# Performance work log

Measured on AMD Instinct MI355X. Metric: run time of the kernel, lower is better.

The kernel has to match this reference:

```python
import jax, jax.numpy as jnp
import numpy as np

K_CENTERS = 10
G_CENTERS = 2
EPS = 1e-12  # tf.math.l2_normalize epsilon


def setup_inputs() -> dict:
    key = jax.random.key(0)
    k1, k2, k3 = jax.random.split(key, 3)
    B, H, W, D = 16, 16, 64, 512
    KC = K_CENTERS + G_CENTERS
    feat = jax.random.normal(k1, (B, H, W, D), dtype=jnp.float32)
    cluster_score = jax.random.normal(k2, (B, H, W, KC), dtype=jnp.float32)
    cluster = jax.random.normal(k3, (KC, D), dtype=jnp.float32)
    return {"feat": feat, "cluster_score": cluster_score, "cluster": cluster}


def reference(feat, cluster_score, cluster):
    B, H, W, D = feat.shape
    KC = cluster.shape[0]
    # Softmax over clusters (stable)
    A = jax.nn.softmax(cluster_score, axis=-1)            # [B,H,W,KC]
    # Flatten spatial dims: sum_{s} A[b,s,k] * (feat[b,s,d] - cluster[k,d])
    Af = A.reshape(B, H * W, KC)
    ff = feat.reshape(B, H * W, D)
    # = einsum(A, feat) - (sum_s A)[b,k] * cluster[k,d]  (avoids [B,S,KC,D] intermediate)
    cluster_res = jnp.einsum('bsk,bsd->bkd', Af, ff) - Af.sum(axis=1)[..., None] * cluster[None]
    # GhostVLAD: keep only real clusters
    cluster_res = cluster_res[:, :K_CENTERS, :]           # [B,K,D]
    # L2 normalize over feature dim
    sq = jnp.sum(cluster_res * cluster_res, axis=-1, keepdims=True)
    cluster_l2 = cluster_res * jax.lax.rsqrt(jnp.maximum(sq, EPS))
    return cluster_l2.reshape(B, K_CENTERS * D)
```

## Files before the change

kernel.cpp:

```cpp
#include <hip/hip_runtime.h>
#include <hip/hip_bf16.h>


#define B_   16
#define S_   1024
#define D_   512
#define KC_  12
#define K_   10
#define CH_  16
#define SCH_ (S_ / CH_)
#define NT1  512
#define NPAR 4

__global__ __launch_bounds__(NT1) void vlad_accum(
    const float* __restrict__ feat, const float* __restrict__ score,
    float* __restrict__ part, float* __restrict__ asum_part)
{
    const int bid = blockIdx.x;
    const int b = bid / CH_, c = bid % CH_;
    const int s0 = c * SCH_;
    const int tid = threadIdx.x;
    const int par = tid >> 7;
    const int col = tid & 127;

    __shared__ float A[SCH_][KC_];
    __shared__ float red[NPAR - 1][K_ * 4][128];

    if (tid < SCH_) {
        const float4* sp = (const float4*)(score + (size_t)(b * S_ + s0 + tid) * KC_);
        const float4 w0 = sp[0], w1 = sp[1], w2 = sp[2];
        float x[KC_] = {w0.x, w0.y, w0.z, w0.w, w1.x, w1.y, w1.z, w1.w,
                        w2.x, w2.y, w2.z, w2.w};
        float m = x[0];
        #pragma unroll
        for (int k = 1; k < KC_; k++) m = fmaxf(m, x[k]);
        float sum = 0.f;
        #pragma unroll
        for (int k = 0; k < KC_; k++) { x[k] = __expf(x[k] - m); sum += x[k]; }
        const float inv = 1.0f / sum;
        #pragma unroll
        for (int k = 0; k < KC_; k++) A[tid][k] = x[k] * inv;
    }
    __syncthreads();

    if (tid < K_) {
        float v = 0.f;
        #pragma unroll
        for (int s = 0; s < SCH_; s++) v += A[s][tid];
        asum_part[(b * CH_ + c) * K_ + tid] = v;
    }

    float acc[K_][4];
    #pragma unroll
    for (int k = 0; k < K_; k++)
        acc[k][0] = acc[k][1] = acc[k][2] = acc[k][3] = 0.f;

    const float4* fp = (const float4*)(feat + (size_t)(b * S_ + s0) * D_) + col;
    #pragma unroll 8
    for (int i = 0; i < SCH_ / NPAR; i++) {
        const int s = NPAR * i + par;
        const float4 v = fp[(size_t)s * (D_ / 4)];
        const float4 a0 = *(const float4*)(&A[s][0]);
        const float4 a1 = *(const float4*)(&A[s][4]);
        const float2 a2 = *(const float2*)(&A[s][8]);
        const float a[K_] = {a0.x, a0.y, a0.z, a0.w, a1.x, a1.y, a1.z, a1.w,
                             a2.x, a2.y};
        #pragma unroll
        for (int k = 0; k < K_; k++) {
            acc[k][0] += a[k] * v.x;
            acc[k][1] += a[k] * v.y;
            acc[k][2] += a[k] * v.z;
            acc[k][3] += a[k] * v.w;
        }
    }

    if (par) {
        float (* const r)[128] = red[par - 1];
        #pragma unroll
        for (int k = 0; k < K_; k++) {
            r[k * 4 + 0][col] = acc[k][0];
            r[k * 4 + 1][col] = acc[k][1];
            r[k * 4 + 2][col] = acc[k][2];
            r[k * 4 + 3][col] = acc[k][3];
        }
    }
    __syncthreads();
    if (!par) {
        float* pp = part + (((size_t)(b * K_) * CH_ + c) * D_) + col * 4;
        #pragma unroll
        for (int k = 0; k < K_; k++) {
            float v0 = acc[k][0], v1 = acc[k][1], v2 = acc[k][2], v3 = acc[k][3];
            #pragma unroll
            for (int p = 0; p < NPAR - 1; p++) {
                v0 += red[p][k * 4 + 0][col];
                v1 += red[p][k * 4 + 1][col];
                v2 += red[p][k * 4 + 2][col];
                v3 += red[p][k * 4 + 3][col];
            }
            *(float4*)(pp + (size_t)k * CH_ * D_) = make_float4(v0, v1, v2, v3);
        }
    }
}

__global__ __launch_bounds__(256) void vlad_final(
    const float* __restrict__ part, const float* __restrict__ asum_part,
    const float* __restrict__ cluster, float* __restrict__ out)
{
    const int b = blockIdx.x / K_;
    const int k = blockIdx.x % K_;
    const int tid = threadIdx.x;
    const int d = tid * 2;

    const float* base = part + ((size_t)(b * K_ + k) * CH_) * D_ + d;
    float s0 = 0.f, s1 = 0.f;
    #pragma unroll 8
    for (int c = 0; c < CH_; c++) {
        const float2 v = *(const float2*)(base + (size_t)c * D_);
        s0 += v.x; s1 += v.y;
    }
    float asv = 0.f;
    #pragma unroll
    for (int c = 0; c < CH_; c++) asv += asum_part[(b * CH_ + c) * K_ + k];

    const float2 cv = *(const float2*)(cluster + (size_t)k * D_ + d);
    const float r0 = s0 - asv * cv.x;
    const float r1 = s1 - asv * cv.y;

    float sq = r0 * r0 + r1 * r1;
    #pragma unroll
    for (int off = 32; off > 0; off >>= 1) sq += __shfl_down(sq, off, 64);
    __shared__ float wsum[4];
    if ((tid & 63) == 0) wsum[tid >> 6] = sq;
    __syncthreads();
    const float tot = wsum[0] + wsum[1] + wsum[2] + wsum[3];
    const float scale = rsqrtf(fmaxf(tot, 1e-12f));

    *(float2*)(out + (size_t)(b * K_ + k) * D_ + d) =
        make_float2(r0 * scale, r1 * scale);
}

extern "C" void kernel_launch(void* const* d_in, const int* in_sizes, int n_in,
                              void* d_out, int out_size, void* d_ws, size_t ws_size,
                              hipStream_t stream) {
    const float* feat    = (const float*)d_in[0];
    const float* score   = (const float*)d_in[1];
    const float* cluster = (const float*)d_in[2];
    float* out = (float*)d_out;

    float* part      = (float*)d_ws;
    float* asum_part = part + (size_t)B_ * K_ * CH_ * D_;

    vlad_accum<<<B_ * CH_, NT1, 0, stream>>>(feat, score, part, asum_part);
    vlad_final<<<B_ * K_, 256, 0, stream>>>(part, asum_part, cluster, out);
}
```

Before: 79.64 us.

## Fuse accumulate and finalize kernels via cooperative launch with grid sync

Merges the two-kernel pipeline into one cooperative kernel that runs the accumulation phase, does a grid-wide sync, then has the first 160 blocks perform the per-cluster reduction and L2 normalization. This is meant to remove the second kernel launch and the gap between kernels. It adds the cost of a grid barrier and depends on all 256 blocks being co-resident, falling back to the old two launches if the cooperative launch fails.

```diff
diff --git a/kernel.cpp b/kernel.cpp
--- a/kernel.cpp
+++ b/kernel.cpp
@@ -1,5 +1,8 @@
 #include <hip/hip_runtime.h>
 #include <hip/hip_bf16.h>
+#include <hip/hip_cooperative_groups.h>
+
+namespace cg = cooperative_groups;
 
 
 #define B_   16
@@ -12,9 +15,10 @@
 #define NT1  512
 #define NPAR 4
 
-__global__ __launch_bounds__(NT1) void vlad_accum(
+__device__ __forceinline__ void accum_body(
     const float* __restrict__ feat, const float* __restrict__ score,
-    float* __restrict__ part, float* __restrict__ asum_part)
+    float* __restrict__ part, float* __restrict__ asum_part,
+    float (&A)[SCH_][KC_], float (&red)[NPAR - 1][K_ * 4][128])
 {
     const int bid = blockIdx.x;
     const int b = bid / CH_, c = bid % CH_;
@@ -22,9 +26,6 @@
     const int tid = threadIdx.x;
     const int par = tid >> 7;
     const int col = tid & 127;
-
-    __shared__ float A[SCH_][KC_];
-    __shared__ float red[NPAR - 1][K_ * 4][128];
 
     if (tid < SCH_) {
         const float4* sp = (const float4*)(score + (size_t)(b * S_ + s0 + tid) * KC_);
@@ -102,6 +103,59 @@
     }
 }
 
+__global__ __launch_bounds__(NT1) void vlad_all(
+    const float* __restrict__ feat, const float* __restrict__ score,
+    const float* __restrict__ cluster, float* __restrict__ part,
+    float* __restrict__ asum_part, float* __restrict__ out)
+{
+    __shared__ float A[SCH_][KC_];
+    __shared__ float red[NPAR - 1][K_ * 4][128];
+    __shared__ float wsum[NT1 / 64];
+
+    accum_body(feat, score, part, asum_part, A, red);
+
+    cg::this_grid().sync();
+
+    const int blk = blockIdx.x;
+    if (blk < B_ * K_) {
+        const int b = blk / K_;
+        const int k = blk % K_;
+        const int d = threadIdx.x;
+
+        const float* base = part + ((size_t)(b * K_ + k) * CH_) * D_ + d;
+        float s = 0.f;
+        #pragma unroll 8
+        for (int c = 0; c < CH_; c++) s += base[(size_t)c * D_];
+
+        float asv = 0.f;
+        #pragma unroll
+        for (int c = 0; c < CH_; c++) asv += asum_part[(b * CH_ + c) * K_ + k];
+
+        const float r = s - asv * cluster[(size_t)k * D_ + d];
+
+        float sq = r * r;
+        #pragma unroll
+        for (int off = 32; off > 0; off >>= 1) sq += __shfl_down(sq, off, 64);
+        if ((d & 63) == 0) wsum[d >> 6] = sq;
+        __syncthreads();
+        float tot = 0.f;
+        #pragma unroll
+        for (int w = 0; w < NT1 / 64; w++) tot += wsum[w];
+        const float scale = rsqrtf(fmaxf(tot, 1e-12f));
+
+        out[(size_t)(b * K_ + k) * D_ + d] = r * scale;
+    }
+}
+
+__global__ __launch_bounds__(NT1) void vlad_accum(
+    const float* __restrict__ feat, const float* __restrict__ score,
+    float* __restrict__ part, float* __restrict__ asum_part)
+{
+    __shared__ float A[SCH_][KC_];
+    __shared__ float red[NPAR - 1][K_ * 4][128];
+    accum_body(feat, score, part, asum_part, A, red);
+}
+
 __global__ __launch_bounds__(256) void vlad_final(
     const float* __restrict__ part, const float* __restrict__ asum_part,
     const float* __restrict__ cluster, float* __restrict__ out)
@@ -150,6 +204,12 @@
     float* part      = (float*)d_ws;
     float* asum_part = part + (size_t)B_ * K_ * CH_ * D_;
 
-    vlad_accum<<<B_ * CH_, NT1, 0, stream>>>(feat, score, part, asum_part);
-    vlad_final<<<B_ * K_, 256, 0, stream>>>(part, asum_part, cluster, out);
-}
+    void* args[] = {(void*)&feat, (void*)&score, (void*)&cluster,
+                    (void*)&part, (void*)&asum_part, (void*)&out};
+    hipError_t err = hipLaunchCooperativeKernel(
+        (const void*)vlad_all, dim3(B_ * CH_), dim3(NT1), args, 0, stream);
+    if (err != hipSuccess) {
+        vlad_accum<<<B_ * CH_, NT1, 0, stream>>>(feat, score, part, asum_part);
+        vlad_final<<<B_ * K_, 256, 0, stream>>>(part, asum_part, cluster, out);
+    }
+}
```

New measurement: 127.5 us. +60.1%, slower.
